# Optimization experiments

Measured on AMD Instinct MI355X. Metric: run time of the kernel, lower is better.

The kernel has to match this reference:

```python
import jax, jax.numpy as jnp
import numpy as np

EMBED_DIM = 512
NUM_HEADS = 8
EPS = 1e-6


def _feature_map(x):
    # elu(x) + 1
    return jax.nn.elu(x) + 1.0


def setup_inputs() -> dict:
    key = jax.random.key(0)
    ks = jax.random.split(key, 11)
    n, s, e = 8, 8192, EMBED_DIM
    scale = 1.0 / np.sqrt(e)
    inp = {
        "query": jax.random.normal(ks[0], (n, s, e), jnp.float32),
        "key": jax.random.normal(ks[1], (n, s, e), jnp.float32),
        "value": jax.random.normal(ks[2], (n, s, e), jnp.float32),
        "Wq": jax.random.normal(ks[3], (e, e), jnp.float32) * scale,
        "bq": jnp.zeros((e,), jnp.float32),
        "Wk": jax.random.normal(ks[4], (e, e), jnp.float32) * scale,
        "bk": jnp.zeros((e,), jnp.float32),
        "Wv": jax.random.normal(ks[5], (e, e), jnp.float32) * scale,
        "bv": jnp.zeros((e,), jnp.float32),
        "Wo": jax.random.normal(ks[6], (e, e), jnp.float32) * scale,
        "bo": jnp.zeros((e,), jnp.float32),
    }
    return inp


def reference(query, key, value, Wq, bq, Wk, bk, Wv, bv, Wo, bo):
    n, s, e = query.shape
    h = NUM_HEADS
    d = e // h
    # linear projections (torch Linear: x @ W.T + b)
    q = query @ Wq.T + bq
    k = key @ Wk.T + bk
    v = value @ Wv.T + bv
    # split into heads: [n, s, h, d]
    q = q.reshape(n, s, h, d)
    k = k.reshape(n, s, h, d)
    v = v.reshape(n, s, h, d)
    Q = _feature_map(q)
    K = _feature_map(k)
    # KV: [n, h, m, d]
    KV = jnp.einsum('nshd,nshm->nhmd', K, v)
    # normalizer Z: [n, l, h]
    Z = 1.0 / (jnp.einsum('nlhd,nhd->nlh', Q, K.sum(axis=1)) + EPS)
    # output values: [n, l, h, m]
    V = jnp.einsum('nlhd,nhmd,nlh->nlhm', Q, KV, Z)
    V = V.reshape(n, s, e)
    return V @ Wo.T + bo
```

## Files before the change

kernel.cpp:

```cpp
#include <hip/hip_runtime.h>
#include <math.h>

#define EMBED 512
#define SEQ   8192
#define EPS   1e-6f

typedef __attribute__((ext_vector_type(8))) short bf16x8;
typedef __attribute__((ext_vector_type(4))) float f32x4;
typedef unsigned short ushort_t;
typedef unsigned int uint_t;

__device__ __forceinline__ ushort_t f2bf(float x) {
  uint_t b = __float_as_uint(x);
  b += 0x7fff + ((b >> 16) & 1);
  return (ushort_t)(b >> 16);
}
__device__ __forceinline__ float bf2f(ushort_t u) {
  return __uint_as_float(((uint_t)u) << 16);
}
__device__ __forceinline__ float bfhi(uint_t packed) {
  return __uint_as_float(packed & 0xffff0000u);
}
__device__ __forceinline__ float bflo(uint_t packed) {
  return __uint_as_float(packed << 16);
}

#define GLL(srcp, dstp)                                                       \
  __builtin_amdgcn_global_load_lds(                                           \
      (const __attribute__((address_space(1))) void*)(const void*)(srcp),     \
      (__attribute__((address_space(3))) void*)(void*)(dstp), 16, 0, 0)

__global__ void convert_split(const float* __restrict__ x,
                              ushort_t* __restrict__ h,
                              ushort_t* __restrict__ l, int n4) {
  const int stride = gridDim.x * blockDim.x;
  for (int i = blockIdx.x * blockDim.x + threadIdx.x; i < n4; i += stride) {
    float4 v = ((const float4*)x)[i];
    ushort_t h0 = f2bf(v.x), h1 = f2bf(v.y), h2 = f2bf(v.z), h3 = f2bf(v.w);
    ushort_t l0 = f2bf(v.x - bf2f(h0)), l1 = f2bf(v.y - bf2f(h1));
    ushort_t l2 = f2bf(v.z - bf2f(h2)), l3 = f2bf(v.w - bf2f(h3));
    uint2 hv, lv;
    hv.x = (uint_t)h0 | ((uint_t)h1 << 16); hv.y = (uint_t)h2 | ((uint_t)h3 << 16);
    lv.x = (uint_t)l0 | ((uint_t)l1 << 16); lv.y = (uint_t)l2 | ((uint_t)l3 << 16);
    ((uint2*)h)[i] = hv; ((uint2*)l)[i] = lv;
  }
}

template <bool ACT, bool SPLIT_OUT>
__global__ __launch_bounds__(256) void gemm_split(
    const ushort_t* __restrict__ Ah, const ushort_t* __restrict__ Al,
    const ushort_t* __restrict__ Bh, const ushort_t* __restrict__ Bl,
    const float* __restrict__ bias,
    ushort_t* __restrict__ Ch, ushort_t* __restrict__ Cl,
    float* __restrict__ Cf, int M) {
  __shared__ __align__(16) ushort_t lAh[128 * 32];
  __shared__ __align__(16) ushort_t lAl[128 * 32];
  __shared__ __align__(16) ushort_t lBh[128 * 32];
  __shared__ __align__(16) ushort_t lBl[128 * 32];

  const int t = threadIdx.x;
  const int m0 = blockIdx.x * 128;
  const int n0 = blockIdx.y * 128;
  const int w = t >> 6, lane = t & 63;
  const int wr = w >> 1, wc = w & 1;
  const int fl = lane & 15, kb = lane >> 4;

  f32x4 acc[4][4];
#pragma unroll
  for (int mi = 0; mi < 4; ++mi)
#pragma unroll
    for (int ni = 0; ni < 4; ++ni) acc[mi][ni] = (f32x4){0.f, 0.f, 0.f, 0.f};

  for (int kt = 0; kt < EMBED / 32; ++kt) {
#pragma unroll
    for (int j = 0; j < 2; ++j) {
      const int i = t + j * 256;
      const int r = i >> 2, p = i & 3;
      const int c = p ^ ((r >> 1) & 3);
      const size_t ga = (size_t)(m0 + r) * EMBED + kt * 32 + c * 8;
      const size_t gb = (size_t)(n0 + r) * EMBED + kt * 32 + c * 8;
      GLL(&Ah[ga], &lAh[(size_t)i * 8]);
      GLL(&Al[ga], &lAl[(size_t)i * 8]);
      GLL(&Bh[gb], &lBh[(size_t)i * 8]);
      GLL(&Bl[gb], &lBl[(size_t)i * 8]);
    }
    __syncthreads();

    bf16x8 fah[4], fal[4], fbh[4], fbl[4];
#pragma unroll
    for (int mi = 0; mi < 4; ++mi) {
      const int r = wr * 64 + mi * 16 + fl;
      const int p = kb ^ ((r >> 1) & 3);
      const int off = r * 32 + p * 8;
      fah[mi] = *(const bf16x8*)&lAh[off];
      fal[mi] = *(const bf16x8*)&lAl[off];
    }
#pragma unroll
    for (int ni = 0; ni < 4; ++ni) {
      const int r = wc * 64 + ni * 16 + fl;
      const int p = kb ^ ((r >> 1) & 3);
      const int off = r * 32 + p * 8;
      fbh[ni] = *(const bf16x8*)&lBh[off];
      fbl[ni] = *(const bf16x8*)&lBl[off];
    }
#pragma unroll
    for (int mi = 0; mi < 4; ++mi)
#pragma unroll
      for (int ni = 0; ni < 4; ++ni) {
        acc[mi][ni] = __builtin_amdgcn_mfma_f32_16x16x32_bf16(fah[mi], fbh[ni], acc[mi][ni], 0, 0, 0);
        acc[mi][ni] = __builtin_amdgcn_mfma_f32_16x16x32_bf16(fah[mi], fbl[ni], acc[mi][ni], 0, 0, 0);
        acc[mi][ni] = __builtin_amdgcn_mfma_f32_16x16x32_bf16(fal[mi], fbh[ni], acc[mi][ni], 0, 0, 0);
      }
    __syncthreads();
  }

  const int rq = lane >> 4;
#pragma unroll
  for (int mi = 0; mi < 4; ++mi)
#pragma unroll
    for (int ni = 0; ni < 4; ++ni) {
      const int col = n0 + wc * 64 + ni * 16 + fl;
      const float bv = bias[col];
#pragma unroll
      for (int q = 0; q < 4; ++q) {
        const int row = m0 + wr * 64 + mi * 16 + rq * 4 + q;
        float v = acc[mi][ni][q] + bv;
        if (ACT) v = (v > 0.f) ? (v + 1.f) : __expf(v);
        const size_t g = (size_t)row * EMBED + col;
        if (SPLIT_OUT) {
          const ushort_t hh = f2bf(v);
          Ch[g] = hh;
          Cl[g] = f2bf(v - bf2f(hh));
        } else {
          Cf[g] = v;
        }
      }
    }
}

__global__ __launch_bounds__(256) void kv_kernel(
    const ushort_t* __restrict__ Kh, const ushort_t* __restrict__ Kl,
    const ushort_t* __restrict__ Vh, const ushort_t* __restrict__ Vl,
    float* __restrict__ KV, float* __restrict__ Ksum) {
  const int nh = blockIdx.x;
  const int n = nh >> 3, h = nh & 7;
  const int sbeg = blockIdx.y * 256;
  __shared__ float Ks[32][64];
  __shared__ float Vs[32][64];
  const int t = threadIdx.x;
  const int ty = t >> 4, tx = t & 15;
  float acc[4][4] = {};
  float ks[4] = {};

  for (int s0 = 0; s0 < 256; s0 += 32) {
#pragma unroll
    for (int i = 0; i < 2; ++i) {
      const int f = t + i * 256;
      const int r = f >> 4, cg = (f & 15) * 4;
      const size_t g = ((size_t)(n * SEQ + sbeg + s0 + r)) * EMBED + h * 64 + cg;
      uint2 kh = *(const uint2*)&Kh[g], kl = *(const uint2*)&Kl[g];
      uint2 vh = *(const uint2*)&Vh[g], vl = *(const uint2*)&Vl[g];
      Ks[r][cg + 0] = bflo(kh.x) + bflo(kl.x);
      Ks[r][cg + 1] = bfhi(kh.x) + bfhi(kl.x);
      Ks[r][cg + 2] = bflo(kh.y) + bflo(kl.y);
      Ks[r][cg + 3] = bfhi(kh.y) + bfhi(kl.y);
      Vs[r][cg + 0] = bflo(vh.x) + bflo(vl.x);
      Vs[r][cg + 1] = bfhi(vh.x) + bfhi(vl.x);
      Vs[r][cg + 2] = bflo(vh.y) + bflo(vl.y);
      Vs[r][cg + 3] = bfhi(vh.y) + bfhi(vl.y);
    }
    __syncthreads();
#pragma unroll 8
    for (int s = 0; s < 32; ++s) {
      float4 vv = *(float4*)&Vs[s][ty * 4];
      float4 kk = *(float4*)&Ks[s][tx * 4];
      float v4[4] = {vv.x, vv.y, vv.z, vv.w};
      float k4[4] = {kk.x, kk.y, kk.z, kk.w};
#pragma unroll
      for (int i = 0; i < 4; ++i)
#pragma unroll
        for (int j = 0; j < 4; ++j) acc[i][j] = fmaf(v4[i], k4[j], acc[i][j]);
      if (ty == 0) {
#pragma unroll
        for (int j = 0; j < 4; ++j) ks[j] += k4[j];
      }
    }
    __syncthreads();
  }
  float* kvb = &KV[(size_t)nh * 4096];
#pragma unroll
  for (int i = 0; i < 4; ++i)
#pragma unroll
    for (int j = 0; j < 4; ++j)
      atomicAdd(&kvb[(ty * 4 + i) * 64 + tx * 4 + j], acc[i][j]);
  if (ty == 0) {
#pragma unroll
    for (int j = 0; j < 4; ++j) atomicAdd(&Ksum[nh * 64 + tx * 4 + j], ks[j]);
  }
}

__global__ __launch_bounds__(256) void prep_b2(
    const float* __restrict__ KV, const float* __restrict__ Ksum,
    ushort_t* __restrict__ B2h, ushort_t* __restrict__ B2l) {
  const int nh = blockIdx.x;
  for (int idx = threadIdx.x; idx < 80 * 64; idx += 256) {
    const int r = idx >> 6, d = idx & 63;
    float val = 0.f;
    if (r < 64) val = KV[(size_t)nh * 4096 + r * 64 + d];
    else if (r == 64) val = Ksum[nh * 64 + d];
    const ushort_t hh = f2bf(val);
    B2h[(size_t)nh * 5120 + idx] = hh;
    B2l[(size_t)nh * 5120 + idx] = f2bf(val - bf2f(hh));
  }
}

__global__ __launch_bounds__(256) void stage3_gemm(
    const ushort_t* __restrict__ Qh, const ushort_t* __restrict__ Ql,
    const ushort_t* __restrict__ B2h, const ushort_t* __restrict__ B2l,
    ushort_t* __restrict__ VoH, ushort_t* __restrict__ VoL) {
  __shared__ __align__(16) ushort_t lAh[128 * 64];
  __shared__ __align__(16) ushort_t lAl[128 * 64];
  const int t = threadIdx.x;
  const int nh = blockIdx.y;
  const int n = nh >> 3, h = nh & 7;
  const int l0 = blockIdx.x * 128;
  const int w = t >> 6, lane = t & 63;
  const int fl = lane & 15, kb = lane >> 4;

#pragma unroll
  for (int j = 0; j < 4; ++j) {
    const int i = t + j * 256;
    const int r = i >> 3, p = i & 7;
    const int c = p ^ (r & 7);
    const size_t g = (size_t)(n * SEQ + l0 + r) * EMBED + h * 64 + c * 8;
    GLL(&Qh[g], &lAh[(size_t)i * 8]);
    GLL(&Ql[g], &lAl[(size_t)i * 8]);
  }

  bf16x8 fbh[2][5], fbl[2][5];
#pragma unroll
  for (int ks = 0; ks < 2; ++ks)
#pragma unroll
    for (int ni = 0; ni < 5; ++ni) {
      const size_t g = (size_t)nh * 5120 + (ni * 16 + fl) * 64 + ks * 32 + kb * 8;
      fbh[ks][ni] = *(const bf16x8*)&B2h[g];
      fbl[ks][ni] = *(const bf16x8*)&B2l[g];
    }

  f32x4 acc[2][5];
#pragma unroll
  for (int mi = 0; mi < 2; ++mi)
#pragma unroll
    for (int ni = 0; ni < 5; ++ni) acc[mi][ni] = (f32x4){0.f, 0.f, 0.f, 0.f};

  __syncthreads();

#pragma unroll
  for (int ks = 0; ks < 2; ++ks) {
    bf16x8 fah[2], fal[2];
#pragma unroll
    for (int mi = 0; mi < 2; ++mi) {
      const int r = w * 32 + mi * 16 + fl;
      const int c = ks * 4 + kb;
      const int p = c ^ (r & 7);
      const int off = r * 64 + p * 8;
      fah[mi] = *(const bf16x8*)&lAh[off];
      fal[mi] = *(const bf16x8*)&lAl[off];
    }
#pragma unroll
    for (int mi = 0; mi < 2; ++mi)
#pragma unroll
      for (int ni = 0; ni < 5; ++ni) {
        acc[mi][ni] = __builtin_amdgcn_mfma_f32_16x16x32_bf16(fah[mi], fbh[ks][ni], acc[mi][ni], 0, 0, 0);
        acc[mi][ni] = __builtin_amdgcn_mfma_f32_16x16x32_bf16(fah[mi], fbl[ks][ni], acc[mi][ni], 0, 0, 0);
        acc[mi][ni] = __builtin_amdgcn_mfma_f32_16x16x32_bf16(fal[mi], fbh[ks][ni], acc[mi][ni], 0, 0, 0);
      }
  }

  const int rq = lane >> 4;
#pragma unroll
  for (int mi = 0; mi < 2; ++mi) {
    float zin[4];
#pragma unroll
    for (int q = 0; q < 4; ++q) {
      const float den = __shfl(acc[mi][4][q], lane & 48);
      zin[q] = 1.f / (den + EPS);
    }
#pragma unroll
    for (int ni = 0; ni < 4; ++ni)
#pragma unroll
      for (int q = 0; q < 4; ++q) {
        const int row = l0 + w * 32 + mi * 16 + rq * 4 + q;
        const int col = h * 64 + ni * 16 + fl;
        const float v = acc[mi][ni][q] * zin[q];
        const size_t g = (size_t)(n * SEQ + row) * EMBED + col;
        const ushort_t hh = f2bf(v);
        VoH[g] = hh;
        VoL[g] = f2bf(v - bf2f(hh));
      }
  }
}

extern "C" void kernel_launch(void* const* d_in, const int* in_sizes, int n_in,
                              void* d_out, int out_size, void* d_ws,
                              size_t ws_size, hipStream_t stream) {
  const float* query = (const float*)d_in[0];
  const float* key   = (const float*)d_in[1];
  const float* value = (const float*)d_in[2];
  const float* Wq = (const float*)d_in[3];
  const float* bq = (const float*)d_in[4];
  const float* Wk = (const float*)d_in[5];
  const float* bk = (const float*)d_in[6];
  const float* Wv = (const float*)d_in[7];
  const float* bv = (const float*)d_in[8];
  const float* Wo = (const float*)d_in[9];
  const float* bo = (const float*)d_in[10];

  const int M = in_sizes[0] / EMBED;
  const size_t ME = (size_t)M * EMBED;

  ushort_t* S1h = (ushort_t*)d_ws;  ushort_t* S1l = S1h + ME;
  ushort_t* S2h = S1h + 2 * ME;     ushort_t* S2l = S1h + 3 * ME;
  ushort_t* S3h = S1h + 4 * ME;     ushort_t* S3l = S1h + 5 * ME;
  float* KV   = (float*)(S1h + 6 * ME);
  float* Ksum = KV + 64 * 64 * 64;
  ushort_t* Wh = (ushort_t*)(Ksum + 64 * 64);
  ushort_t* Wl = Wh + (size_t)EMBED * EMBED;
  ushort_t* B2h = S1h;
  ushort_t* B2l = S1h + (size_t)64 * 5120;

  hipMemsetAsync(KV, 0, (64 * 64 * 64 + 64 * 64) * sizeof(float), stream);

  const int n4big = (int)(ME / 4);
  const int n4w = EMBED * EMBED / 4;
  dim3 gg(M / 128, EMBED / 128);

  convert_split<<<2048, 256, 0, stream>>>(key, S1h, S1l, n4big);
  convert_split<<<256, 256, 0, stream>>>(Wk, Wh, Wl, n4w);
  gemm_split<true, true><<<gg, 256, 0, stream>>>(S1h, S1l, Wh, Wl, bk, S2h, S2l, nullptr, M);

  convert_split<<<2048, 256, 0, stream>>>(value, S1h, S1l, n4big);
  convert_split<<<256, 256, 0, stream>>>(Wv, Wh, Wl, n4w);
  gemm_split<false, true><<<gg, 256, 0, stream>>>(S1h, S1l, Wh, Wl, bv, S3h, S3l, nullptr, M);

  kv_kernel<<<dim3(64, 32), 256, 0, stream>>>(S2h, S2l, S3h, S3l, KV, Ksum);

  convert_split<<<2048, 256, 0, stream>>>(query, S1h, S1l, n4big);
  convert_split<<<256, 256, 0, stream>>>(Wq, Wh, Wl, n4w);
  gemm_split<true, true><<<gg, 256, 0, stream>>>(S1h, S1l, Wh, Wl, bq, S2h, S2l, nullptr, M);

  prep_b2<<<64, 256, 0, stream>>>(KV, Ksum, B2h, B2l);
  stage3_gemm<<<dim3(SEQ / 128, 64), 256, 0, stream>>>(S2h, S2l, B2h, B2l, S3h, S3l);

  convert_split<<<256, 256, 0, stream>>>(Wo, Wh, Wl, n4w);
  gemm_split<false, false><<<gg, 256, 0, stream>>>(S3h, S3l, Wh, Wl, bo, nullptr, nullptr, (float*)d_out, M);
}
```

Before: 1.220 ms.

## Fuse fp32-to-bf16 split conversion into GEMM A-tile loads and keep intermediates fp32

Removes the separate convert_split passes over the large activation tensors. GEMMs and the stage-3 kernel now read fp32 A directly and split it into hi/lo bf16 in registers before storing to LDS. Intermediates are stored as fp32 rather than hi/lo bf16 pairs, and the KV kernel now double-buffers its fp32 loads with global_load_lds. Grid dimensions are swapped so that blocks sharing the same A rows run adjacently. This cuts several full-tensor read/write passes, at the cost of more conversion ALU work inside the GEMM loops and synchronous global loads for A.

```diff
diff --git a/kernel.cpp b/kernel.cpp
--- a/kernel.cpp
+++ b/kernel.cpp
@@ -18,11 +18,14 @@
 __device__ __forceinline__ float bf2f(ushort_t u) {
   return __uint_as_float(((uint_t)u) << 16);
 }
-__device__ __forceinline__ float bfhi(uint_t packed) {
-  return __uint_as_float(packed & 0xffff0000u);
-}
-__device__ __forceinline__ float bflo(uint_t packed) {
-  return __uint_as_float(packed << 16);
+
+__device__ __forceinline__ void split8(const float* av, bf16x8& hv, bf16x8& lv) {
+#pragma unroll
+  for (int e = 0; e < 8; ++e) {
+    const ushort_t hh = f2bf(av[e]);
+    hv[e] = (short)hh;
+    lv[e] = (short)f2bf(av[e] - bf2f(hh));
+  }
 }
 
 #define GLL(srcp, dstp)                                                       \
@@ -46,21 +49,19 @@
   }
 }
 
-template <bool ACT, bool SPLIT_OUT>
-__global__ __launch_bounds__(256) void gemm_split(
-    const ushort_t* __restrict__ Ah, const ushort_t* __restrict__ Al,
-    const ushort_t* __restrict__ Bh, const ushort_t* __restrict__ Bl,
-    const float* __restrict__ bias,
-    ushort_t* __restrict__ Ch, ushort_t* __restrict__ Cl,
-    float* __restrict__ Cf, int M) {
+template <bool ACT>
+__global__ __launch_bounds__(256) void gemm_f32A(
+    const float* __restrict__ A, const ushort_t* __restrict__ Bh,
+    const ushort_t* __restrict__ Bl, const float* __restrict__ bias,
+    float* __restrict__ C, int M) {
   __shared__ __align__(16) ushort_t lAh[128 * 32];
   __shared__ __align__(16) ushort_t lAl[128 * 32];
   __shared__ __align__(16) ushort_t lBh[128 * 32];
   __shared__ __align__(16) ushort_t lBl[128 * 32];
 
   const int t = threadIdx.x;
-  const int m0 = blockIdx.x * 128;
-  const int n0 = blockIdx.y * 128;
+  const int n0 = blockIdx.x * 128;
+  const int m0 = blockIdx.y * 128;
   const int w = t >> 6, lane = t & 63;
   const int wr = w >> 1, wc = w & 1;
   const int fl = lane & 15, kb = lane >> 4;
@@ -77,12 +78,24 @@
       const int i = t + j * 256;
       const int r = i >> 2, p = i & 3;
       const int c = p ^ ((r >> 1) & 3);
-      const size_t ga = (size_t)(m0 + r) * EMBED + kt * 32 + c * 8;
       const size_t gb = (size_t)(n0 + r) * EMBED + kt * 32 + c * 8;
-      GLL(&Ah[ga], &lAh[(size_t)i * 8]);
-      GLL(&Al[ga], &lAl[(size_t)i * 8]);
       GLL(&Bh[gb], &lBh[(size_t)i * 8]);
       GLL(&Bl[gb], &lBl[(size_t)i * 8]);
+    }
+#pragma unroll
+    for (int j = 0; j < 2; ++j) {
+      const int i = t + j * 256;
+      const int r = i >> 2, c8 = i & 3;
+      const float* ap = &A[(size_t)(m0 + r) * EMBED + kt * 32 + c8 * 8];
+      float av[8];
+      *(float4*)&av[0] = *(const float4*)ap;
+      *(float4*)&av[4] = *(const float4*)(ap + 4);
+      bf16x8 hv, lv;
+      split8(av, hv, lv);
+      const int p = c8 ^ ((r >> 1) & 3);
+      const int off = r * 32 + p * 8;
+      *(bf16x8*)&lAh[off] = hv;
+      *(bf16x8*)&lAl[off] = lv;
     }
     __syncthreads();
 
@@ -126,54 +139,51 @@
         const int row = m0 + wr * 64 + mi * 16 + rq * 4 + q;
         float v = acc[mi][ni][q] + bv;
         if (ACT) v = (v > 0.f) ? (v + 1.f) : __expf(v);
-        const size_t g = (size_t)row * EMBED + col;
-        if (SPLIT_OUT) {
-          const ushort_t hh = f2bf(v);
-          Ch[g] = hh;
-          Cl[g] = f2bf(v - bf2f(hh));
-        } else {
-          Cf[g] = v;
-        }
-      }
-    }
-}
-
-__global__ __launch_bounds__(256) void kv_kernel(
-    const ushort_t* __restrict__ Kh, const ushort_t* __restrict__ Kl,
-    const ushort_t* __restrict__ Vh, const ushort_t* __restrict__ Vl,
+        C[(size_t)row * EMBED + col] = v;
+      }
+    }
+}
+
+__global__ __launch_bounds__(256) void kv_f32(
+    const float* __restrict__ Kf, const float* __restrict__ Vf,
     float* __restrict__ KV, float* __restrict__ Ksum) {
   const int nh = blockIdx.x;
   const int n = nh >> 3, h = nh & 7;
   const int sbeg = blockIdx.y * 256;
-  __shared__ float Ks[32][64];
-  __shared__ float Vs[32][64];
+  __shared__ __align__(16) float Ks[2][32][64];
+  __shared__ __align__(16) float Vs[2][32][64];
   const int t = threadIdx.x;
   const int ty = t >> 4, tx = t & 15;
   float acc[4][4] = {};
   float ks[4] = {};
 
-  for (int s0 = 0; s0 < 256; s0 += 32) {
-#pragma unroll
-    for (int i = 0; i < 2; ++i) {
-      const int f = t + i * 256;
-      const int r = f >> 4, cg = (f & 15) * 4;
-      const size_t g = ((size_t)(n * SEQ + sbeg + s0 + r)) * EMBED + h * 64 + cg;
-      uint2 kh = *(const uint2*)&Kh[g], kl = *(const uint2*)&Kl[g];
-      uint2 vh = *(const uint2*)&Vh[g], vl = *(const uint2*)&Vl[g];
-      Ks[r][cg + 0] = bflo(kh.x) + bflo(kl.x);
-      Ks[r][cg + 1] = bfhi(kh.x) + bfhi(kl.x);
-      Ks[r][cg + 2] = bflo(kh.y) + bflo(kl.y);
-      Ks[r][cg + 3] = bfhi(kh.y) + bfhi(kl.y);
-      Vs[r][cg + 0] = bflo(vh.x) + bflo(vl.x);
-      Vs[r][cg + 1] = bfhi(vh.x) + bfhi(vl.x);
-      Vs[r][cg + 2] = bflo(vh.y) + bflo(vl.y);
-      Vs[r][cg + 3] = bfhi(vh.y) + bfhi(vl.y);
-    }
-    __syncthreads();
+#pragma unroll
+  for (int j = 0; j < 2; ++j) {
+    const int i = t + j * 256;
+    const int r = i >> 4, c4 = (i & 15) * 4;
+    const size_t g = ((size_t)(n * SEQ + sbeg + r)) * EMBED + h * 64 + c4;
+    GLL(&Kf[g], &Ks[0][r][c4]);
+    GLL(&Vf[g], &Vs[0][r][c4]);
+  }
+  __syncthreads();
+
+  int buf = 0;
+  for (int c = 0; c < 8; ++c) {
+    if (c < 7) {
+#pragma unroll
+      for (int j = 0; j < 2; ++j) {
+        const int i = t + j * 256;
+        const int r = i >> 4, c4 = (i & 15) * 4;
+        const size_t g =
+            ((size_t)(n * SEQ + sbeg + (c + 1) * 32 + r)) * EMBED + h * 64 + c4;
+        GLL(&Kf[g], &Ks[buf ^ 1][r][c4]);
+        GLL(&Vf[g], &Vs[buf ^ 1][r][c4]);
+      }
+    }
 #pragma unroll 8
     for (int s = 0; s < 32; ++s) {
-      float4 vv = *(float4*)&Vs[s][ty * 4];
-      float4 kk = *(float4*)&Ks[s][tx * 4];
+      float4 vv = *(float4*)&Vs[buf][s][ty * 4];
+      float4 kk = *(float4*)&Ks[buf][s][tx * 4];
       float v4[4] = {vv.x, vv.y, vv.z, vv.w};
       float k4[4] = {kk.x, kk.y, kk.z, kk.w};
 #pragma unroll
@@ -186,7 +196,9 @@
       }
     }
     __syncthreads();
-  }
+    buf ^= 1;
+  }
+
   float* kvb = &KV[(size_t)nh * 4096];
 #pragma unroll
   for (int i = 0; i < 4; ++i)
@@ -214,27 +226,32 @@
   }
 }
 
-__global__ __launch_bounds__(256) void stage3_gemm(
-    const ushort_t* __restrict__ Qh, const ushort_t* __restrict__ Ql,
-    const ushort_t* __restrict__ B2h, const ushort_t* __restrict__ B2l,
-    ushort_t* __restrict__ VoH, ushort_t* __restrict__ VoL) {
+__global__ __launch_bounds__(256) void stage3_f32A(
+    const float* __restrict__ Qf, const ushort_t* __restrict__ B2h,
+    const ushort_t* __restrict__ B2l, float* __restrict__ Vo) {
   __shared__ __align__(16) ushort_t lAh[128 * 64];
   __shared__ __align__(16) ushort_t lAl[128 * 64];
   const int t = threadIdx.x;
-  const int nh = blockIdx.y;
+  const int nh = blockIdx.x;
   const int n = nh >> 3, h = nh & 7;
-  const int l0 = blockIdx.x * 128;
+  const int l0 = blockIdx.y * 128;
   const int w = t >> 6, lane = t & 63;
   const int fl = lane & 15, kb = lane >> 4;
 
 #pragma unroll
   for (int j = 0; j < 4; ++j) {
     const int i = t + j * 256;
-    const int r = i >> 3, p = i & 7;
-    const int c = p ^ (r & 7);
-    const size_t g = (size_t)(n * SEQ + l0 + r) * EMBED + h * 64 + c * 8;
-    GLL(&Qh[g], &lAh[(size_t)i * 8]);
-    GLL(&Ql[g], &lAl[(size_t)i * 8]);
+    const int r = i >> 3, c8 = i & 7;
+    const float* qp = &Qf[(size_t)(n * SEQ + l0 + r) * EMBED + h * 64 + c8 * 8];
+    float av[8];
+    *(float4*)&av[0] = *(const float4*)qp;
+    *(float4*)&av[4] = *(const float4*)(qp + 4);
+    bf16x8 hv, lv;
+    split8(av, hv, lv);
+    const int p = c8 ^ (r & 7);
+    const int off = r * 64 + p * 8;
+    *(bf16x8*)&lAh[off] = hv;
+    *(bf16x8*)&lAl[off] = lv;
   }
 
   bf16x8 fbh[2][5], fbl[2][5];
@@ -292,11 +309,7 @@
       for (int q = 0; q < 4; ++q) {
         const int row = l0 + w * 32 + mi * 16 + rq * 4 + q;
         const int col = h * 64 + ni * 16 + fl;
-        const float v = acc[mi][ni][q] * zin[q];
-        const size_t g = (size_t)(n * SEQ + row) * EMBED + col;
-        const ushort_t hh = f2bf(v);
-        VoH[g] = hh;
-        VoL[g] = f2bf(v - bf2f(hh));
+        Vo[(size_t)(n * SEQ + row) * EMBED + col] = acc[mi][ni][q] * zin[q];
       }
   }
 }
@@ -319,39 +332,34 @@
   const int M = in_sizes[0] / EMBED;
   const size_t ME = (size_t)M * EMBED;
 
-  ushort_t* S1h = (ushort_t*)d_ws;  ushort_t* S1l = S1h + ME;
-  ushort_t* S2h = S1h + 2 * ME;     ushort_t* S2l = S1h + 3 * ME;
-  ushort_t* S3h = S1h + 4 * ME;     ushort_t* S3l = S1h + 5 * ME;
-  float* KV   = (float*)(S1h + 6 * ME);
+  float* S1 = (float*)d_ws;
+  float* S2 = S1 + ME;
+  float* KV = S2 + ME;
   float* Ksum = KV + 64 * 64 * 64;
   ushort_t* Wh = (ushort_t*)(Ksum + 64 * 64);
   ushort_t* Wl = Wh + (size_t)EMBED * EMBED;
-  ushort_t* B2h = S1h;
-  ushort_t* B2l = S1h + (size_t)64 * 5120;
+  ushort_t* B2h = Wl + (size_t)EMBED * EMBED;
+  ushort_t* B2l = B2h + (size_t)64 * 5120;
 
   hipMemsetAsync(KV, 0, (64 * 64 * 64 + 64 * 64) * sizeof(float), stream);
 
-  const int n4big = (int)(ME / 4);
   const int n4w = EMBED * EMBED / 4;
-  dim3 gg(M / 128, EMBED / 128);
-
-  convert_split<<<2048, 256, 0, stream>>>(key, S1h, S1l, n4big);
+  dim3 gg(EMBED / 128, M / 128);
+
   convert_split<<<256, 256, 0, stream>>>(Wk, Wh, Wl, n4w);
-  gemm_split<true, true><<<gg, 256, 0, stream>>>(S1h, S1l, Wh, Wl, bk, S2h, S2l, nullptr, M);
-
-  convert_split<<<2048, 256, 0, stream>>>(value, S1h, S1l, n4big);
+  gemm_f32A<true><<<gg, 256, 0, stream>>>(key, Wh, Wl, bk, S1, M);
+
   convert_split<<<256, 256, 0, stream>>>(Wv, Wh, Wl, n4w);
-  gemm_split<false, true><<<gg, 256, 0, stream>>>(S1h, S1l, Wh, Wl, bv, S3h, S3l, nullptr, M);
-
-  kv_kernel<<<dim3(64, 32), 256, 0, stream>>>(S2h, S2l, S3h, S3l, KV, Ksum);
-
-  convert_split<<<2048, 256, 0, stream>>>(query, S1h, S1l, n4big);
+  gemm_f32A<false><<<gg, 256, 0, stream>>>(value, Wh, Wl, bv, S2, M);
+
+  kv_f32<<<dim3(64, 32), 256, 0, stream>>>(S1, S2, KV, Ksum);
+
   convert_split<<<256, 256, 0, stream>>>(Wq, Wh, Wl, n4w);
-  gemm_split<true, true><<<gg, 256, 0, stream>>>(S1h, S1l, Wh, Wl, bq, S2h, S2l, nullptr, M);
+  gemm_f32A<true><<<gg, 256, 0, stream>>>(query, Wh, Wl, bq, S1, M);
 
   prep_b2<<<64, 256, 0, stream>>>(KV, Ksum, B2h, B2l);
-  stage3_gemm<<<dim3(SEQ / 128, 64), 256, 0, stream>>>(S2h, S2l, B2h, B2l, S3h, S3l);
+  stage3_f32A<<<dim3(64, SEQ / 128), 256, 0, stream>>>(S1, B2h, B2l, S2);
 
   convert_split<<<256, 256, 0, stream>>>(Wo, Wh, Wl, n4w);
-  gemm_split<false, false><<<gg, 256, 0, stream>>>(S3h, S3l, Wh, Wl, bo, nullptr, nullptr, (float*)d_out, M);
-}
+  gemm_f32A<false><<<gg, 256, 0, stream>>>(S2, Wh, Wl, bo, (float*)d_out, M);
+}
```

Result: faster. 1.105 ms (-9.4%).
